# Performance work log

Hardware: AMD Instinct MI355X
Metric: run time of the kernel (lower is better)

The kernel has to match this reference:

```python
import jax, jax.numpy as jnp
import numpy as np

HEADS = 16
HEAD_DIM = 64  # embed_size 1024 // 16


def setup_inputs() -> dict:
    key = jax.random.key(0)
    ks = jax.random.split(key, 6)
    N, S, E = 2, 2048, 1024
    return {
        "values": jax.random.normal(ks[0], (N, S, E), dtype=jnp.float32),
        "keys": jax.random.normal(ks[1], (N, S, E), dtype=jnp.float32),
        "queries": jax.random.normal(ks[2], (N, S, E), dtype=jnp.float32),
        "Wv": jax.random.normal(ks[3], (E, E), dtype=jnp.float32) * (E ** -0.5),
        "Wk": jax.random.normal(ks[4], (E, E), dtype=jnp.float32) * (E ** -0.5),
        "Wq": jax.random.normal(ks[5], (E, E), dtype=jnp.float32) * (E ** -0.5),
    }


def reference(values, keys, queries, Wv, Wk, Wq):
    N, Sq, E = queries.shape
    Sk = keys.shape[1]
    H, D = HEADS, HEAD_DIM
    # linear projections (torch Linear: x @ W^T), then split heads
    v = (values @ Wv.T).reshape(N, Sk, H, D)
    k = (keys @ Wk.T).reshape(N, Sk, H, D)
    q = (queries @ Wq.T).reshape(N, Sq, H, D)
    # QK^T -> [N, H, Q, K]
    scores = jnp.einsum("nqhd,nkhd->nhqk", q, k)
    # no mask (original forward takes mask=None path); scale by sqrt(head_dim)
    attn = jax.nn.softmax(scores / jnp.asarray(D, scores.dtype) ** 0.5, axis=-1)
    # AV -> [N, Q, H, D] -> [N, Q, E]; note: fc_out is never applied in the original forward
    out = jnp.einsum("nhql,nlhd->nqhd", attn, v).reshape(N, Sq, H * D)
    return out
```

## Files before the change

kernel.cpp:

```cpp
#include <hip/hip_runtime.h>
#include <math.h>

#define SEQ 2048
#define EMB 1024
#define NH  16
#define HD  64

typedef __attribute__((ext_vector_type(8))) short short8;
typedef __attribute__((ext_vector_type(4))) float f32x4;

static const size_t XE = (size_t)2 * SEQ * EMB;
static const size_t WE = (size_t)EMB * EMB;

static __device__ __forceinline__ short f2bf(float f) {
    unsigned u = __builtin_bit_cast(unsigned, f);
    u = u + 0x7fffu + ((u >> 16) & 1u);
    return (short)(u >> 16);
}

#if __has_builtin(__builtin_amdgcn_cvt_pk_bf16_f32)
typedef __attribute__((ext_vector_type(2))) __bf16 bf16x2;
static __device__ __forceinline__ unsigned pk2(float a, float b) {
    bf16x2 v = __builtin_amdgcn_cvt_pk_bf16_f32(a, b);
    return __builtin_bit_cast(unsigned, v);
}
#else
static __device__ __forceinline__ unsigned pk2(float a, float b) {
    return (unsigned)(unsigned short)f2bf(a) |
           ((unsigned)(unsigned short)f2bf(b) << 16);
}
#endif

static __device__ __forceinline__ short8 cvt8(float4 a, float4 b) {
    union { unsigned u[4]; short8 s; } r;
    r.u[0] = pk2(a.x, a.y); r.u[1] = pk2(a.z, a.w);
    r.u[2] = pk2(b.x, b.y); r.u[3] = pk2(b.z, b.w);
    return r.s;
}

static __device__ __forceinline__ void gload16(const void* g, void* l) {
    __builtin_amdgcn_global_load_lds(
        (const __attribute__((address_space(1))) void*)g,
        (__attribute__((address_space(3))) void*)l, 16, 0, 0);
}

__global__ __launch_bounds__(256)
void cvt_all(const float* __restrict__ xq, const float* __restrict__ xk,
             const float* __restrict__ xv, const float* __restrict__ wq,
             const float* __restrict__ wk, const float* __restrict__ wv,
             short* __restrict__ dxq, short* __restrict__ dxk,
             short* __restrict__ dxv, short* __restrict__ dw) {
    int id = blockIdx.x;
    const float* s; short* d; size_t i;
    if (id < 6144) {
        int seg = id >> 11, o = id & 2047;
        s = (seg == 0) ? xq : (seg == 1) ? xk : xv;
        d = (seg == 0) ? dxq : (seg == 1) ? dxk : dxv;
        i = (size_t)o * 256 + threadIdx.x;
    } else {
        int wid = id - 6144;
        int seg = wid >> 9, o = wid & 511;
        s = (seg == 0) ? wq : (seg == 1) ? wk : wv;
        d = dw + (size_t)seg * WE;
        i = (size_t)o * 256 + threadIdx.x;
    }
    const float4* sp = (const float4*)s;
    float4 a = sp[2 * i], b = sp[2 * i + 1];
    *(short8*)(d + i * 8) = cvt8(a, b);
}

#define ES_STRIDE 136
__global__ __launch_bounds__(512, 4)
void proj(const short* __restrict__ Xq, const short* __restrict__ Xk,
          const short* __restrict__ Xv, const short* __restrict__ Wb,
          short* __restrict__ qb, short* __restrict__ kbuf,
          short* __restrict__ vt) {
    __shared__ __align__(16) char lds_raw[65536];
    short8* Fs = (short8*)lds_raw;
    short8* Hs = (short8*)(lds_raw + 32768);
    short*  Es = (short*)lds_raw;

    const int L = blockIdx.x;
    const int xcd = L & 7, i = L >> 3;
    const int z = i >> 5;
    const int m = i & 31;
    const int ty = xcd * 4 + (m & 3);
    const int tx = m >> 2;

    const short* Fop; const short* Hop; short* C;
    if (z == 0)      { Fop = Xq; Hop = Wb;           C = qb;   }
    else if (z == 1) { Fop = Xk; Hop = Wb + WE;      C = kbuf; }
    else             { Fop = Xv; Hop = Wb + 2 * WE;  C = vt;   }
    const int fr0 = ty * 128;
    const int hr0 = tx * 128;

    const int t = threadIdx.x, w = t >> 6, lane = t & 63;
    const int l15 = lane & 15, quad = lane >> 4;
    const int lr3 = lane >> 3, lc7 = lane & 7;
    const int mh = (w >> 2) * 64;
    const int nh = (w & 3) * 32;

    auto stageF = [&](int pp, int k0) {
#pragma unroll
        for (int j = 0; j < 2; ++j) {
            int rb = j * 64 + w * 8;
            gload16(Fop + (size_t)(fr0 + rb + lr3) * EMB + k0 + ((lc7 ^ lr3) * 8),
                    &Fs[pp * 1024 + rb * 8]);
        }
    };
    auto stageH = [&](int pp, int k0) {
#pragma unroll
        for (int j = 0; j < 2; ++j) {
            int rb = j * 64 + w * 8;
            gload16(Hop + (size_t)(hr0 + rb + lr3) * EMB + k0 + ((lc7 ^ lr3) * 8),
                    &Hs[pp * 1024 + rb * 8]);
        }
    };

    f32x4 acc[4][2];
#pragma unroll
    for (int a = 0; a < 4; ++a)
#pragma unroll
        for (int b = 0; b < 2; ++b) acc[a][b] = 0.f;

    stageF(0, 0);
    stageH(0, 0);

    int p = 0;
    for (int k0 = 0; k0 < EMB; k0 += 64, p ^= 1) {
        __syncthreads();
        if (k0 + 64 < EMB) { stageF(p ^ 1, k0 + 64); stageH(p ^ 1, k0 + 64); }

#pragma unroll
        for (int kb2 = 0; kb2 < 2; ++kb2) {
            short8 af[4], bf[2];
            int cx = (kb2 * 4 + quad) ^ (l15 & 7);
            if (z < 2) {
#pragma unroll
                for (int mi = 0; mi < 4; ++mi)
                    af[mi] = Fs[p * 1024 + (mh + mi * 16 + l15) * 8 + cx];
#pragma unroll
                for (int ni = 0; ni < 2; ++ni)
                    bf[ni] = Hs[p * 1024 + (nh + ni * 16 + l15) * 8 + cx];
            } else {
#pragma unroll
                for (int mi = 0; mi < 4; ++mi)
                    af[mi] = Hs[p * 1024 + (mh + mi * 16 + l15) * 8 + cx];
#pragma unroll
                for (int ni = 0; ni < 2; ++ni)
                    bf[ni] = Fs[p * 1024 + (nh + ni * 16 + l15) * 8 + cx];
            }
#pragma unroll
            for (int mi = 0; mi < 4; ++mi)
#pragma unroll
                for (int ni = 0; ni < 2; ++ni)
                    acc[mi][ni] = __builtin_amdgcn_mfma_f32_16x16x32_bf16(
                        af[mi], bf[ni], acc[mi][ni], 0, 0, 0);
        }
    }

    __syncthreads();
#pragma unroll
    for (int mi = 0; mi < 4; ++mi)
#pragma unroll
        for (int ni = 0; ni < 2; ++ni)
#pragma unroll
            for (int r = 0; r < 4; ++r) {
                int lr_ = mh + mi * 16 + quad * 4 + r;
                int lc_ = nh + ni * 16 + l15;
                Es[lr_ * ES_STRIDE + lc_] = f2bf(acc[mi][ni][r]);
            }
    __syncthreads();
    {
        int row = t >> 2, q4 = t & 3;
        const short* src = Es + row * ES_STRIDE + q4 * 32;
        short* dst;
        if (z < 2) {
            dst = C + (size_t)(fr0 + row) * EMB + hr0 + q4 * 32;
        } else {
            int bz = fr0 >> 11, s0 = fr0 & 2047;
            dst = C + ((size_t)bz * EMB + hr0 + row) * SEQ + s0 + q4 * 32;
        }
#pragma unroll
        for (int j = 0; j < 4; ++j)
            *(short8*)(dst + j * 8) = *(const short8*)(src + j * 8);
    }
}

__global__ __launch_bounds__(256, 2)
void attn_mfma(const short* __restrict__ Qg, const short* __restrict__ Kg,
               const short* __restrict__ Vtg, float* __restrict__ OutD) {
    __shared__ short8 QPs[1024];
    __shared__ short8 Ks[3][512];
    __shared__ short8 Vs[3][512];

    const int t = threadIdx.x, w = t >> 6, lane = t & 63;
    const int l15 = lane & 15, quad = lane >> 4;
    const int lr3 = lane >> 3, lc7 = lane & 7;
    const int L = blockIdx.x;
    const int xcd = L & 7, i = L >> 3;
    const int bh = xcd * 4 + (i & 3);
    const int q0 = (i >> 2) * 128;
    const int b = bh >> 4, h = bh & 15;
    const short* Qb = Qg + (size_t)b * SEQ * EMB + h * HD;
    const short* Kb = Kg + (size_t)b * SEQ * EMB + h * HD;
    const short* Vb = Vtg + ((size_t)b * EMB + h * HD) * SEQ;

    auto stageKV = [&](int p, int kt) {
#pragma unroll
        for (int j = 0; j < 2; ++j) {
            int rb = w * 16 + j * 8;
            int r = rb + lr3;
            gload16(Kb + (size_t)(kt + r) * EMB + ((lc7 ^ lr3) * 8),
                    &Ks[p][rb * 8]);
            gload16(Vb + (size_t)r * SEQ + kt + ((lc7 ^ lr3) * 8),
                    &Vs[p][rb * 8]);
        }
    };

#pragma unroll
    for (int j = 0; j < 4; ++j) {
        int rb = w * 32 + j * 8;
        gload16(Qb + (size_t)(q0 + rb + lr3) * EMB + ((lc7 ^ lr3) * 8),
                &QPs[rb * 8]);
    }
    stageKV(0, 0);
    stageKV(1, 64);
    asm volatile("s_waitcnt vmcnt(4)" ::: "memory");
    __builtin_amdgcn_s_barrier();
    __builtin_amdgcn_sched_barrier(0);

    short8 qf[2][2];
#pragma unroll
    for (int qi = 0; qi < 2; ++qi)
#pragma unroll
        for (int kb2 = 0; kb2 < 2; ++kb2) {
            int row = w * 32 + qi * 16 + l15;
            qf[qi][kb2] = QPs[row * 8 + ((kb2 * 4 + quad) ^ (l15 & 7))];
        }

    short8 ones8;
#pragma unroll
    for (int j = 0; j < 8; ++j) ones8[j] = (short)0x3F80;

    f32x4 o[2][4];
    f32x4 ol[2];
#pragma unroll
    for (int qi = 0; qi < 2; ++qi) {
        ol[qi] = 0.f;
#pragma unroll
        for (int ni = 0; ni < 4; ++ni) o[qi][ni] = 0.f;
    }
    const float cl2 = 0.18033688011112042f;
    const float c0  = 11.541560327111707f;

    int p = 0;
    for (int kt = 0; kt < SEQ; kt += 64) {
        if (kt) {
            if (kt + 64 < SEQ) {
                asm volatile("s_waitcnt vmcnt(4)" ::: "memory");
            } else {
                asm volatile("s_waitcnt vmcnt(0)" ::: "memory");
            }
            __builtin_amdgcn_s_barrier();
            __builtin_amdgcn_sched_barrier(0);
        }
        if (kt + 128 < SEQ) {
            int pn = p + 2; if (pn >= 3) pn -= 3;
            stageKV(pn, kt + 128);
        }

        f32x4 s[4][2];
#pragma unroll
        for (int kblk = 0; kblk < 4; ++kblk)
#pragma unroll
            for (int qi = 0; qi < 2; ++qi) s[kblk][qi] = 0.f;
#pragma unroll
        for (int kb2 = 0; kb2 < 2; ++kb2) {
            short8 ak[4];
#pragma unroll
            for (int kblk = 0; kblk < 4; ++kblk) {
                int row = kblk * 16 + l15;
                ak[kblk] = Ks[p][row * 8 + ((kb2 * 4 + quad) ^ (l15 & 7))];
            }
            __builtin_amdgcn_s_setprio(1);
#pragma unroll
            for (int kblk = 0; kblk < 4; ++kblk)
#pragma unroll
                for (int qi = 0; qi < 2; ++qi)
                    s[kblk][qi] = __builtin_amdgcn_mfma_f32_16x16x32_bf16(
                        ak[kblk], qf[qi][kb2], s[kblk][qi], 0, 0, 0);
            __builtin_amdgcn_s_setprio(0);
        }

#pragma unroll
        for (int qi = 0; qi < 2; ++qi) {
            int row = w * 32 + qi * 16 + l15;
#pragma unroll
            for (int kblk = 0; kblk < 4; ++kblk) {
                float p0 = __builtin_amdgcn_exp2f(fmaf(s[kblk][qi][0], cl2, -c0));
                float p1 = __builtin_amdgcn_exp2f(fmaf(s[kblk][qi][1], cl2, -c0));
                float p2 = __builtin_amdgcn_exp2f(fmaf(s[kblk][qi][2], cl2, -c0));
                float p3 = __builtin_amdgcn_exp2f(fmaf(s[kblk][qi][3], cl2, -c0));
                uint2 pv; pv.x = pk2(p0, p1); pv.y = pk2(p2, p3);
                int kc = kblk * 2 + (quad >> 1);
                *(uint2*)((char*)QPs +
                    (((row * 8 + (kc ^ (l15 & 7))) << 4) | ((quad & 1) << 3)))
                    = pv;
            }
        }

#pragma unroll
        for (int kb2 = 0; kb2 < 2; ++kb2) {
            short8 ap[2], bv[4];
#pragma unroll
            for (int qi = 0; qi < 2; ++qi) {
                int row = w * 32 + qi * 16 + l15;
                ap[qi] = QPs[row * 8 + ((kb2 * 4 + quad) ^ (l15 & 7))];
            }
#pragma unroll
            for (int ni = 0; ni < 4; ++ni) {
                int dr = ni * 16 + l15;
                bv[ni] = Vs[p][dr * 8 + ((kb2 * 4 + quad) ^ (l15 & 7))];
            }
            __builtin_amdgcn_s_setprio(1);
#pragma unroll
            for (int qi = 0; qi < 2; ++qi) {
#pragma unroll
                for (int ni = 0; ni < 4; ++ni)
                    o[qi][ni] = __builtin_amdgcn_mfma_f32_16x16x32_bf16(
                        ap[qi], bv[ni], o[qi][ni], 0, 0, 0);
                ol[qi] = __builtin_amdgcn_mfma_f32_16x16x32_bf16(
                    ap[qi], ones8, ol[qi], 0, 0, 0);
            }
            __builtin_amdgcn_s_setprio(0);
        }

        p = (p + 1 == 3) ? 0 : p + 1;
    }

#pragma unroll
    for (int qi = 0; qi < 2; ++qi)
#pragma unroll
        for (int r = 0; r < 4; ++r) {
            float inv = 1.0f / ol[qi][r];
            int q = q0 + w * 32 + qi * 16 + quad * 4 + r;
            float* op = OutD + ((size_t)b * SEQ + q) * EMB + h * HD;
#pragma unroll
            for (int ni = 0; ni < 4; ++ni)
                op[ni * 16 + l15] = o[qi][ni][r] * inv;
        }
}

extern "C" void kernel_launch(void* const* d_in, const int* in_sizes, int n_in,
                              void* d_out, int out_size, void* d_ws, size_t ws_size,
                              hipStream_t stream) {
    const float* values  = (const float*)d_in[0];
    const float* keys    = (const float*)d_in[1];
    const float* queries = (const float*)d_in[2];
    const float* Wv      = (const float*)d_in[3];
    const float* Wk      = (const float*)d_in[4];
    const float* Wq      = (const float*)d_in[5];
    float* out = (float*)d_out;

    short* qb  = (short*)d_ws;
    short* kb  = qb + XE;
    short* vt  = kb + XE;
    short* wb  = vt + XE;
    short* xqb = wb + 3 * WE;
    short* xkb = xqb + XE;
    short* xvb = xkb + XE;

    cvt_all<<<7680, 256, 0, stream>>>(queries, keys, values, Wq, Wk, Wv,
                                      xqb, xkb, xvb, wb);
    proj<<<768, 512, 0, stream>>>(xqb, xkb, xvb, wb, qb, kb, vt);
    attn_mfma<<<512, 256, 0, stream>>>(qb, kb, vt, out);
}
```

Before: 197.7 us.

## Restructure projection GEMM to 256 threads with 64x64 warp tiles and K=32 stages

The projection kernel moves from 512 threads, each wave computing 64x32, to 256 threads, each wave computing 64x64 (4x4 MFMA tiles). The K step drops from 64 to 32, and LDS shrinks to about 34KB with an unswizzled row layout. Larger per-wave tiles raise MFMA-to-LDS-load reuse and lower LDS use, which may let more blocks fit per CU. In exchange, dropping the XOR swizzle risks LDS bank conflicts, and the shorter K step means twice as many barriers.

```diff
diff --git a/kernel.cpp b/kernel.cpp
--- a/kernel.cpp
+++ b/kernel.cpp
@@ -70,14 +70,14 @@
 }
 
 #define ES_STRIDE 136
-__global__ __launch_bounds__(512, 4)
+__global__ __launch_bounds__(256, 4)
 void proj(const short* __restrict__ Xq, const short* __restrict__ Xk,
           const short* __restrict__ Xv, const short* __restrict__ Wb,
           short* __restrict__ qb, short* __restrict__ kbuf,
           short* __restrict__ vt) {
-    __shared__ __align__(16) char lds_raw[65536];
+    __shared__ __align__(16) char lds_raw[34816];
     short8* Fs = (short8*)lds_raw;
-    short8* Hs = (short8*)(lds_raw + 32768);
+    short8* Hs = (short8*)(lds_raw + 16384);
     short*  Es = (short*)lds_raw;
 
     const int L = blockIdx.x;
@@ -96,66 +96,66 @@
 
     const int t = threadIdx.x, w = t >> 6, lane = t & 63;
     const int l15 = lane & 15, quad = lane >> 4;
-    const int lr3 = lane >> 3, lc7 = lane & 7;
-    const int mh = (w >> 2) * 64;
-    const int nh = (w & 3) * 32;
+    const int lr4 = lane >> 2, lc3 = lane & 3;
+    const int wr = w >> 1, wc = w & 1;
+    const int mh = wr * 64, nh = wc * 64;
 
     auto stageF = [&](int pp, int k0) {
 #pragma unroll
         for (int j = 0; j < 2; ++j) {
-            int rb = j * 64 + w * 8;
-            gload16(Fop + (size_t)(fr0 + rb + lr3) * EMB + k0 + ((lc7 ^ lr3) * 8),
-                    &Fs[pp * 1024 + rb * 8]);
+            int row = w * 32 + j * 16 + lr4;
+            gload16(Fop + (size_t)(fr0 + row) * EMB + k0 + lc3 * 8,
+                    &Fs[pp * 512 + w * 128 + j * 64]);
         }
     };
     auto stageH = [&](int pp, int k0) {
 #pragma unroll
         for (int j = 0; j < 2; ++j) {
-            int rb = j * 64 + w * 8;
-            gload16(Hop + (size_t)(hr0 + rb + lr3) * EMB + k0 + ((lc7 ^ lr3) * 8),
-                    &Hs[pp * 1024 + rb * 8]);
+            int row = w * 32 + j * 16 + lr4;
+            gload16(Hop + (size_t)(hr0 + row) * EMB + k0 + lc3 * 8,
+                    &Hs[pp * 512 + w * 128 + j * 64]);
         }
     };
 
-    f32x4 acc[4][2];
+    f32x4 acc[4][4];
 #pragma unroll
     for (int a = 0; a < 4; ++a)
 #pragma unroll
-        for (int b = 0; b < 2; ++b) acc[a][b] = 0.f;
+        for (int b = 0; b < 4; ++b) acc[a][b] = 0.f;
 
     stageF(0, 0);
     stageH(0, 0);
 
     int p = 0;
-    for (int k0 = 0; k0 < EMB; k0 += 64, p ^= 1) {
+    for (int k0 = 0; k0 < EMB; k0 += 32, p ^= 1) {
         __syncthreads();
-        if (k0 + 64 < EMB) { stageF(p ^ 1, k0 + 64); stageH(p ^ 1, k0 + 64); }
-
-#pragma unroll
-        for (int kb2 = 0; kb2 < 2; ++kb2) {
-            short8 af[4], bf[2];
-            int cx = (kb2 * 4 + quad) ^ (l15 & 7);
-            if (z < 2) {
-#pragma unroll
-                for (int mi = 0; mi < 4; ++mi)
-                    af[mi] = Fs[p * 1024 + (mh + mi * 16 + l15) * 8 + cx];
-#pragma unroll
-                for (int ni = 0; ni < 2; ++ni)
-                    bf[ni] = Hs[p * 1024 + (nh + ni * 16 + l15) * 8 + cx];
-            } else {
-#pragma unroll
-                for (int mi = 0; mi < 4; ++mi)
-                    af[mi] = Hs[p * 1024 + (mh + mi * 16 + l15) * 8 + cx];
-#pragma unroll
-                for (int ni = 0; ni < 2; ++ni)
-                    bf[ni] = Fs[p * 1024 + (nh + ni * 16 + l15) * 8 + cx];
-            }
-#pragma unroll
-            for (int mi = 0; mi < 4; ++mi)
-#pragma unroll
-                for (int ni = 0; ni < 2; ++ni)
+        if (k0 + 32 < EMB) { stageF(p ^ 1, k0 + 32); stageH(p ^ 1, k0 + 32); }
+
+        short8 bf[4];
+        if (z < 2) {
+#pragma unroll
+            for (int ni = 0; ni < 4; ++ni)
+                bf[ni] = Hs[p * 512 + (nh + ni * 16 + l15) * 4 + quad];
+#pragma unroll
+            for (int mi = 0; mi < 4; ++mi) {
+                short8 af = Fs[p * 512 + (mh + mi * 16 + l15) * 4 + quad];
+#pragma unroll
+                for (int ni = 0; ni < 4; ++ni)
                     acc[mi][ni] = __builtin_amdgcn_mfma_f32_16x16x32_bf16(
-                        af[mi], bf[ni], acc[mi][ni], 0, 0, 0);
+                        af, bf[ni], acc[mi][ni], 0, 0, 0);
+            }
+        } else {
+#pragma unroll
+            for (int ni = 0; ni < 4; ++ni)
+                bf[ni] = Fs[p * 512 + (nh + ni * 16 + l15) * 4 + quad];
+#pragma unroll
+            for (int mi = 0; mi < 4; ++mi) {
+                short8 af = Hs[p * 512 + (mh + mi * 16 + l15) * 4 + quad];
+#pragma unroll
+                for (int ni = 0; ni < 4; ++ni)
+                    acc[mi][ni] = __builtin_amdgcn_mfma_f32_16x16x32_bf16(
+                        af, bf[ni], acc[mi][ni], 0, 0, 0);
+            }
         }
     }
 
@@ -163,7 +163,7 @@
 #pragma unroll
     for (int mi = 0; mi < 4; ++mi)
 #pragma unroll
-        for (int ni = 0; ni < 2; ++ni)
+        for (int ni = 0; ni < 4; ++ni)
 #pragma unroll
             for (int r = 0; r < 4; ++r) {
                 int lr_ = mh + mi * 16 + quad * 4 + r;
@@ -172,17 +172,17 @@
             }
     __syncthreads();
     {
-        int row = t >> 2, q4 = t & 3;
-        const short* src = Es + row * ES_STRIDE + q4 * 32;
+        int row = t >> 1, half = t & 1;
+        const short* src = Es + row * ES_STRIDE + half * 64;
         short* dst;
         if (z < 2) {
-            dst = C + (size_t)(fr0 + row) * EMB + hr0 + q4 * 32;
+            dst = C + (size_t)(fr0 + row) * EMB + hr0 + half * 64;
         } else {
             int bz = fr0 >> 11, s0 = fr0 & 2047;
-            dst = C + ((size_t)bz * EMB + hr0 + row) * SEQ + s0 + q4 * 32;
-        }
-#pragma unroll
-        for (int j = 0; j < 4; ++j)
+            dst = C + ((size_t)bz * EMB + hr0 + row) * SEQ + s0 + half * 64;
+        }
+#pragma unroll
+        for (int j = 0; j < 8; ++j)
             *(short8*)(dst + j * 8) = *(const short8*)(src + j * 8);
     }
 }
@@ -373,6 +373,6 @@
 
     cvt_all<<<7680, 256, 0, stream>>>(queries, keys, values, Wq, Wk, Wv,
                                       xqb, xkb, xvb, wb);
-    proj<<<768, 512, 0, stream>>>(xqb, xkb, xvb, wb, qb, kb, vt);
+    proj<<<768, 256, 0, stream>>>(xqb, xkb, xvb, wb, qb, kb, vt);
     attn_mfma<<<512, 256, 0, stream>>>(qb, kb, vt, out);
 }
```

After: 325.3 us. 64.5% more time.
